# Performance work log

Measured on AMD Instinct MI355X. Metric: run time of the kernel, lower is better.

The kernel has to match this reference:

```python
import jax, jax.numpy as jnp
import numpy as np

B, T, HID = 1, 256, 2048
H, D = 16, 128
KD = H * D
CONV = 4
MAX_CG = 30
LAMB_LB = 0.25
NORM_EPS = 1e-5


def setup_inputs() -> dict:
    key = jax.random.key(0)
    ks = jax.random.split(key, 10)
    s = 0.02
    init_lamb = float(np.log(np.exp(1.0 - LAMB_LB) - 1.0))  # softplus^-1(1 - lower_bound)
    return {
        "hidden_states": jax.random.normal(ks[0], (B, T, HID), jnp.float32),
        "Wq": jax.random.normal(ks[1], (HID, KD), jnp.float32) * s,
        "Wk": jax.random.normal(ks[2], (HID, KD), jnp.float32) * s,
        "Wv": jax.random.normal(ks[3], (HID, KD), jnp.float32) * s,
        "Wa": jax.random.normal(ks[4], (HID, H), jnp.float32) * s,
        "ba": jnp.full((H,), 2.0, jnp.float32),
        "Wb": jax.random.normal(ks[5], (HID, H), jnp.float32) * s,
        "bb": jnp.zeros((H,), jnp.float32),
        "conv_wq": jax.random.normal(ks[6], (KD, CONV), jnp.float32) * s,
        "conv_wk": jax.random.normal(ks[7], (KD, CONV), jnp.float32) * s,
        "lambda_params": jnp.full((KD,), init_lamb, jnp.float32),
        "o_norm_w": jnp.ones((D,), jnp.float32),
        "Wo": jax.random.normal(ks[8], (KD, HID), jnp.float32) * s,
    }


def short_conv_silu(x, w):
    # depthwise causal conv over time; x [b,t,c], w [c,k]
    k = w.shape[1]
    xp = jnp.pad(x, ((0, 0), (k - 1, 0), (0, 0)))
    t = x.shape[1]
    y = xp[:, 0:t, :] * w[:, 0]
    for i in range(1, k):
        y = y + xp[:, i:i + t, :] * w[:, i]
    return jax.nn.silu(y)


def l2norm(x):
    return x * jax.lax.rsqrt(jnp.sum(x * x, -1, keepdims=True) + 1e-6)


def rmsnorm(x, w):
    return x * jax.lax.rsqrt(jnp.mean(x * x, -1, keepdims=True) + NORM_EPS) * w


def cg_solve(A, b):
    # solve A x = b per (batch, head) with fixed CG iterations, x0 = 0
    matvec = lambda p: jnp.einsum('bhij,bhj->bhi', A, p)
    x0 = jnp.zeros_like(b)
    rs0 = jnp.sum(b * b, -1)

    def body(i, st):
        xc, r, p, rs = st
        Ap = matvec(p)
        alpha = rs / (jnp.sum(p * Ap, -1) + 1e-12)
        xc = xc + alpha[..., None] * p
        r = r - alpha[..., None] * Ap
        rs_n = jnp.sum(r * r, -1)
        p = r + (rs_n / (rs + 1e-12))[..., None] * p
        return xc, r, p, rs_n

    xf, _, _, _ = jax.lax.fori_loop(0, MAX_CG, body, (x0, b, b, rs0))
    return xf


def mesa_recurrence(q, k, v, g, beta, lamb_diag):
    # q,k,v [b,t,h,d]; g,beta [b,t,h]; lamb_diag [h,d,d]
    def step(carry, inp):
        h_kk, h_kv = carry
        qt, kt, vt, gt, bt = inp
        decay = jnp.exp(gt)[..., None, None]
        b_ = bt[..., None, None]
        h_kk = h_kk * decay + b_ * (kt[..., :, None] * kt[..., None, :])
        h_kv = h_kv * decay + b_ * (kt[..., :, None] * vt[..., None, :])
        A = h_kk + lamb_diag[None]
        q_star = cg_solve(A, qt)
        ot = jnp.einsum('bhk,bhkv->bhv', q_star, h_kv)
        return (h_kk, h_kv), ot

    init = (jnp.zeros((B, H, D, D), q.dtype), jnp.zeros((B, H, D, D), q.dtype))
    xs = (q.transpose(1, 0, 2, 3), k.transpose(1, 0, 2, 3), v.transpose(1, 0, 2, 3),
          g.transpose(1, 0, 2), beta.transpose(1, 0, 2))
    _, o = jax.lax.scan(step, init, xs)
    return o.transpose(1, 0, 2, 3)  # [b,t,h,d]


def reference(hidden_states, Wq, Wk, Wv, Wa, ba, Wb, bb, conv_wq, conv_wk,
              lambda_params, o_norm_w, Wo):
    x = hidden_states
    q = short_conv_silu(x @ Wq, conv_wq)
    k = short_conv_silu(x @ Wk, conv_wk)
    v = x @ Wv
    q = l2norm(q.reshape(B, T, H, D))
    k = l2norm(k.reshape(B, T, H, D))
    v = v.reshape(B, T, H, D)
    beta = jax.nn.sigmoid(x @ Wb + bb)          # [b,t,h]
    g = jax.nn.log_sigmoid(x @ Wa + ba)          # [b,t,h]
    lamb = (jax.nn.softplus(lambda_params) + LAMB_LB).reshape(H, D)
    lamb_diag = lamb[:, :, None] * jnp.eye(D, dtype=lamb.dtype)  # [h,d,d]
    o = mesa_recurrence(q, k, v, g, beta, lamb_diag)
    o = rmsnorm(o, o_norm_w)
    o = o.reshape(B, T, KD) @ Wo
    return o
```

## Files before the change

kernel.cpp:

```cpp
#include <hip/hip_runtime.h>
#include <math.h>

#define TT 256
#define HIDDEN 2048
#define NH 16
#define HD 128
#define KDIM 2048
#define NCG 30

typedef _Float16 h4 __attribute__((ext_vector_type(4)));
typedef _Float16 half8 __attribute__((ext_vector_type(8)));
typedef float floatx4 __attribute__((ext_vector_type(4)));

__device__ __forceinline__ half8 cvt8(const float4 x, const float4 y) {
    half8 f;
    f[0] = (_Float16)x.x; f[1] = (_Float16)x.y; f[2] = (_Float16)x.z; f[3] = (_Float16)x.w;
    f[4] = (_Float16)y.x; f[5] = (_Float16)y.y; f[6] = (_Float16)y.z; f[7] = (_Float16)y.w;
    return f;
}

#define ASTR 72
__global__ __launch_bounds__(256) void gemm_kernel(
    const float* __restrict__ A,
    const float* __restrict__ Wq, const float* __restrict__ Wk,
    const float* __restrict__ Wv,
    const float* __restrict__ Wa, const float* __restrict__ Wb,
    float* __restrict__ C0, float* __restrict__ C1, float* __restrict__ C2,
    const float* __restrict__ ba, const float* __restrict__ bb,
    float* __restrict__ g, float* __restrict__ beta)
{
    __shared__ __align__(16) _Float16 Bsh[2][8192];
    __shared__ __align__(16) _Float16 Ash[2][32 * ASTR];

    const int tid = threadIdx.x, lane = tid & 63, w = tid >> 6;
    const int q = lane >> 4, l16 = lane & 15;

    const int b = blockIdx.x;
    const int xcd = b & 7, gslot = b >> 3;
    int nt, mt;
    if (gslot < 48) { nt = xcd * 6 + (gslot >> 3); mt = gslot & 7; }
    else           { nt = 48;                      mt = xcd; }
    const int mat = nt >> 4;
    const int ntile = nt & 15;
    const int n0 = ntile * 128;
    const float* __restrict__ W = (mat == 0) ? Wq : (mat == 1) ? Wk : (mat == 2) ? Wv : Wa;
    float* __restrict__ C = (mat == 0) ? C0 : (mat == 1) ? C1 : C2;
    const int m0 = mt * 32;
    const int kt2 = w >> 1;

    const int ar = tid >> 3, ac = (tid & 7) * 8;
    const float* __restrict__ Ap = &A[(size_t)(m0 + ar) * KDIM + ac];

    floatx4 acc[2][2] = {};
    float4 ax, ay;
    float bwv[2][16];
    float bab[16];

    auto loadB = [&](int s) {
        const float* base = &W[(size_t)(s * 64 + w * 16) * KDIM + n0 + lane];
#pragma unroll
        for (int i = 0; i < 16; i++) {
            bwv[0][i] = base[(size_t)i * KDIM];
            bwv[1][i] = base[(size_t)i * KDIM + 64];
        }
    };
    auto writeB = [&](int buf) {
#pragma unroll
        for (int hf = 0; hf < 2; hf++)
#pragma unroll
            for (int kg = 0; kg < 2; kg++) {
                const int kc = (w * 2 + kg) & 3;
                half8 h;
#pragma unroll
                for (int j = 0; j < 8; j++) h[j] = (_Float16)bwv[hf][kg * 8 + j];
                *(half8*)&Bsh[buf][((kt2 * 4 + kc) * 128 + hf * 64 + lane) * 8] = h;
            }
    };
    auto loadBab = [&](int s) {
        if (w >= 2) return;
        const float* __restrict__ Wsrc = (w == 0) ? Wa : Wb;
        const int hh = lane & 15, ko = lane >> 4;
#pragma unroll
        for (int hf = 0; hf < 2; hf++)
#pragma unroll
            for (int j = 0; j < 8; j++)
                bab[hf * 8 + j] = Wsrc[(size_t)(s * 64 + hf * 32 + ko * 8 + j) * NH + hh];
    };
    auto writeBab = [&](int buf) {
        if (w >= 2) return;
        const int hh = lane & 15, ko = lane >> 4;
        const int nn = w * 16 + hh;
#pragma unroll
        for (int hf = 0; hf < 2; hf++) {
            half8 h;
#pragma unroll
            for (int j = 0; j < 8; j++) h[j] = (_Float16)bab[hf * 8 + j];
            *(half8*)&Bsh[buf][((hf * 4 + ko) * 128 + nn) * 8] = h;
        }
    };

    if (mat == 3) {
        half8 z = {};
#pragma unroll
        for (int i = 0; i < 6; i++) {
            const int idx = i * 256 + tid;
            const int buf = idx & 1;
            const int rest = idx >> 1;
            const int slot = rest / 96, nrel = rest - slot * 96;
            *(half8*)&Bsh[buf][(slot * 128 + 32 + nrel) * 8] = z;
        }
        loadBab(0); writeBab(0); loadBab(1);
    } else {
        loadB(0); writeB(0); loadB(1);
    }
    ax = *(const float4*)&Ap[0]; ay = *(const float4*)&Ap[4];
    *(half8*)&Ash[0][ar * ASTR + ac] = cvt8(ax, ay);
    ax = *(const float4*)&Ap[64]; ay = *(const float4*)&Ap[68];
    __syncthreads();

    const int NSTEP = KDIM / 64;
    for (int s = 0; s < NSTEP; s++) {
        const int cur = s & 1;
#pragma unroll
        for (int kk = 0; kk < 2; kk++) {
            const half8 bf0 = *(const half8*)&Bsh[cur][kk * 4096 + q * 1024 + (w * 32 + l16) * 8];
            const half8 bf1 = *(const half8*)&Bsh[cur][kk * 4096 + q * 1024 + (w * 32 + 16 + l16) * 8];
            const half8 af0 = *(const half8*)&Ash[cur][l16 * ASTR + kk * 32 + q * 8];
            const half8 af1 = *(const half8*)&Ash[cur][(16 + l16) * ASTR + kk * 32 + q * 8];
            acc[0][0] = __builtin_amdgcn_mfma_f32_16x16x32_f16(af0, bf0, acc[0][0], 0, 0, 0);
            acc[0][1] = __builtin_amdgcn_mfma_f32_16x16x32_f16(af0, bf1, acc[0][1], 0, 0, 0);
            acc[1][0] = __builtin_amdgcn_mfma_f32_16x16x32_f16(af1, bf0, acc[1][0], 0, 0, 0);
            acc[1][1] = __builtin_amdgcn_mfma_f32_16x16x32_f16(af1, bf1, acc[1][1], 0, 0, 0);
        }
        if (s + 1 < NSTEP) {
            if (mat == 3) {
                writeBab(cur ^ 1);
                if (s + 2 < NSTEP) loadBab(s + 2);
            } else {
                writeB(cur ^ 1);
                if (s + 2 < NSTEP) loadB(s + 2);
            }
            *(half8*)&Ash[cur ^ 1][ar * ASTR + ac] = cvt8(ax, ay);
            if (s + 2 < NSTEP) {
                ax = *(const float4*)&Ap[(s + 2) * 64];
                ay = *(const float4*)&Ap[(s + 2) * 64 + 4];
            }
        }
        __syncthreads();
    }

    if (mat == 3) {
        if (w == 0) {
            const float bav = ba[l16], bbv = bb[l16];
#pragma unroll
            for (int r = 0; r < 4; r++) {
                const int t0r = m0 + q * 4 + r, t1r = m0 + 16 + q * 4 + r;
                float z0 = acc[0][0][r] + bav;
                g[t0r * NH + l16] = fminf(z0, 0.f) - log1pf(__expf(-fabsf(z0)));
                float z1 = acc[0][1][r] + bbv;
                beta[t0r * NH + l16] = 1.f / (1.f + __expf(-z1));
                float z2 = acc[1][0][r] + bav;
                g[t1r * NH + l16] = fminf(z2, 0.f) - log1pf(__expf(-fabsf(z2)));
                float z3 = acc[1][1][r] + bbv;
                beta[t1r * NH + l16] = 1.f / (1.f + __expf(-z3));
            }
        }
        return;
    }

#pragma unroll
    for (int r = 0; r < 4; r++) {
        C[(size_t)(m0 + q * 4 + r) * KDIM + n0 + w * 32 + l16] = acc[0][0][r];
        C[(size_t)(m0 + q * 4 + r) * KDIM + n0 + w * 32 + 16 + l16] = acc[0][1][r];
        C[(size_t)(m0 + 16 + q * 4 + r) * KDIM + n0 + w * 32 + l16] = acc[1][0][r];
        C[(size_t)(m0 + 16 + q * 4 + r) * KDIM + n0 + w * 32 + 16 + l16] = acc[1][1][r];
    }
}

__global__ __launch_bounds__(256) void gemm64_kernel(
    const float* __restrict__ A, const float* __restrict__ Wo,
    float* __restrict__ C)
{
    __shared__ __align__(16) _Float16 Bsh[2][4096];
    __shared__ __align__(16) _Float16 Ash[2][32 * ASTR];

    const int tid = threadIdx.x, lane = tid & 63, w = tid >> 6;
    const int q = lane >> 4, l16 = lane & 15;
    const int b = blockIdx.x;
    const int xcd = b & 7, gslot = b >> 3;
    const int nt = xcd * 4 + (gslot >> 3), mt = gslot & 7;
    const int n0 = nt * 64, m0 = mt * 32;
    const int kt2 = w >> 1;

    const int ar = tid >> 3, ac = (tid & 7) * 8;
    const float* __restrict__ Ap = &A[(size_t)(m0 + ar) * KDIM + ac];

    floatx4 acc0 = {}, acc1 = {};
    float4 ax, ay;
    float bwv[16];

    auto loadB = [&](int s) {
        const float* base = &Wo[(size_t)(s * 64 + w * 16) * KDIM + n0 + lane];
#pragma unroll
        for (int i = 0; i < 16; i++) bwv[i] = base[(size_t)i * KDIM];
    };
    auto writeB = [&](int buf) {
#pragma unroll
        for (int kg = 0; kg < 2; kg++) {
            const int kc = (w * 2 + kg) & 3;
            half8 h;
#pragma unroll
            for (int j = 0; j < 8; j++) h[j] = (_Float16)bwv[kg * 8 + j];
            *(half8*)&Bsh[buf][((kt2 * 4 + kc) * 64 + lane) * 8] = h;
        }
    };

    loadB(0); writeB(0); loadB(1);
    ax = *(const float4*)&Ap[0]; ay = *(const float4*)&Ap[4];
    *(half8*)&Ash[0][ar * ASTR + ac] = cvt8(ax, ay);
    ax = *(const float4*)&Ap[64]; ay = *(const float4*)&Ap[68];
    __syncthreads();

    const int NSTEP = KDIM / 64;
    for (int s = 0; s < NSTEP; s++) {
        const int cur = s & 1;
#pragma unroll
        for (int kk = 0; kk < 2; kk++) {
            const half8 bf  = *(const half8*)&Bsh[cur][kk * 2048 + q * 512 + (w * 16 + l16) * 8];
            const half8 af0 = *(const half8*)&Ash[cur][l16 * ASTR + kk * 32 + q * 8];
            const half8 af1 = *(const half8*)&Ash[cur][(16 + l16) * ASTR + kk * 32 + q * 8];
            acc0 = __builtin_amdgcn_mfma_f32_16x16x32_f16(af0, bf, acc0, 0, 0, 0);
            acc1 = __builtin_amdgcn_mfma_f32_16x16x32_f16(af1, bf, acc1, 0, 0, 0);
        }
        if (s + 1 < NSTEP) {
            writeB(cur ^ 1);
            if (s + 2 < NSTEP) loadB(s + 2);
            *(half8*)&Ash[cur ^ 1][ar * ASTR + ac] = cvt8(ax, ay);
            if (s + 2 < NSTEP) {
                ax = *(const float4*)&Ap[(s + 2) * 64];
                ay = *(const float4*)&Ap[(s + 2) * 64 + 4];
            }
        }
        __syncthreads();
    }

#pragma unroll
    for (int r = 0; r < 4; r++) {
        C[(size_t)(m0 + q * 4 + r) * KDIM + n0 + w * 16 + l16] = acc0[r];
        C[(size_t)(m0 + 16 + q * 4 + r) * KDIM + n0 + w * 16 + l16] = acc1[r];
    }
}

__global__ __launch_bounds__(256) void conv_silu_l2_kernel(
    const float* __restrict__ q_pre, const float* __restrict__ k_pre,
    const float* __restrict__ cwq, const float* __restrict__ cwk,
    float* __restrict__ qn, float* __restrict__ kn)
{
    const int t = blockIdx.x, h = blockIdx.y;
    const int which = threadIdx.x >> 7, d = threadIdx.x & 127;
    const int w = threadIdx.x >> 6;
    const int c = h * HD + d;
    const float* pre = which ? k_pre : q_pre;
    const float* cw  = which ? cwk : cwq;
    float y = 0.f;
#pragma unroll
    for (int i = 0; i < 4; i++) {
        const int ts = t - 3 + i;
        if (ts >= 0) y = fmaf(pre[ts * KDIM + c], cw[c * 4 + i], y);
    }
    const float s = y / (1.f + __expf(-y));
    float v = s * s;
#pragma unroll
    for (int off = 32; off > 0; off >>= 1) v += __shfl_down(v, off, 64);
    __shared__ float red[4];
    if ((threadIdx.x & 63) == 0) red[w] = v;
    __syncthreads();
    const float sum = red[which * 2] + red[which * 2 + 1];
    float* dst = which ? kn : qn;
    dst[t * KDIM + c] = s * rsqrtf(sum + 1e-6f);
}

#define PSTR 136
#define YSTR 264

template<int SMAX>
__device__ __forceinline__ void mesa_cg(
    const float* __restrict__ qn, const float* __restrict__ kn, const float* __restrict__ vv,
    const float* __restrict__ g, const float* __restrict__ bet, const float* __restrict__ lp,
    const float* __restrict__ onw, float* __restrict__ out,
    int h, int t0, _Float16* Psh, _Float16* Ysh, float* red,
    float* Gsh, float* bets)
{
    constexpr int NSUB1 = SMAX / 64;
    constexpr int NK2   = SMAX / 32;

    const int tid = threadIdx.x, lane = tid & 63, w = tid >> 6;
    const int quad = lane >> 4, l16 = lane & 15;
    const int tmy = t0 + l16;
    const int dbase = w * 32;

    {
        float sc = g[tid * NH + h];
#pragma unroll
        for (int off = 1; off < 64; off <<= 1) {
            const float o = __shfl_up(sc, off, 64);
            if (lane >= off) sc += o;
        }
        if (lane == 63) red[w] = sc;
        bets[tid] = bet[tid * NH + h];
        __syncthreads();
        float woff = 0.f;
        for (int u = 0; u < w; u++) woff += red[u];
        Gsh[tid] = sc + woff;
        __syncthreads();
    }

    half8 K1[NSUB1][4];
#pragma unroll
    for (int ii = 0; ii < NSUB1; ii++) {
        const int srow = 16 * (w + 4 * ii) + l16;
        const float* kp = &kn[(srow * NH + h) * HD];
#pragma unroll
        for (int kk = 0; kk < 4; kk++) {
            const float4 a = *(const float4*)&kp[kk * 32 + quad * 8];
            const float4 b = *(const float4*)&kp[kk * 32 + quad * 8 + 4];
            K1[ii][kk] = cvt8(a, b);
        }
    }

    half8 KtF[2][NK2];
#pragma unroll
    for (int ss = 0; ss < 2; ss++) {
        const int d = dbase + ss * 16 + l16;
#pragma unroll
        for (int kk = 0; kk < NK2; kk++) {
#pragma unroll
            for (int j = 0; j < 8; j++) {
                const int s = kk * 32 + quad * 8 + j;
                KtF[ss][kk][j] = (_Float16)kn[(s * NH + h) * HD + d];
            }
        }
    }

    half8 Vf[NK2][2];
#pragma unroll
    for (int kk = 0; kk < NK2; kk++) {
#pragma unroll
        for (int ss = 0; ss < 2; ss++) {
            const int dv = dbase + ss * 16 + l16;
#pragma unroll
            for (int j = 0; j < 8; j++) {
                const int s = kk * 32 + quad * 8 + j;
                Vf[kk][ss][j] = (_Float16)vv[(s * NH + h) * HD + dv];
            }
        }
    }

    const float Gt = Gsh[tmy];
    float Wm[NSUB1][4];
#pragma unroll
    for (int ii = 0; ii < NSUB1; ii++)
#pragma unroll
        for (int r = 0; r < 4; r++) {
            const int s = 16 * (w + 4 * ii) + quad * 4 + r;
            Wm[ii][r] = (s <= tmy) ? bets[s] * __expf(Gt - Gsh[s]) : 0.f;
        }
    float lam[8], xv[8], rv[8], pv[8];
#pragma unroll
    for (int ss = 0; ss < 2; ss++)
#pragma unroll
        for (int r = 0; r < 4; r++) {
            const int e = ss * 4 + r;
            const int d = dbase + ss * 16 + quad * 4 + r;
            const float lx = lp[h * HD + d];
            lam[e] = fmaxf(lx, 0.f) + log1pf(__expf(-fabsf(lx))) + 0.25f;
            const float b = qn[(tmy * NH + h) * HD + d];
            xv[e] = 0.f; rv[e] = b; pv[e] = b;
        }
    float rs = 0.f;
#pragma unroll
    for (int e = 0; e < 8; e++) rs += rv[e] * rv[e];
    rs += __shfl_xor(rs, 16, 64); rs += __shfl_xor(rs, 32, 64);

    auto writeP = [&](const float* src) {
#pragma unroll
        for (int ss = 0; ss < 2; ss++) {
            h4 ph;
            ph.x = (_Float16)src[ss * 4 + 0]; ph.y = (_Float16)src[ss * 4 + 1];
            ph.z = (_Float16)src[ss * 4 + 2]; ph.w = (_Float16)src[ss * 4 + 3];
            *(h4*)&Psh[l16 * PSTR + dbase + ss * 16 + quad * 4] = ph;
        }
    };
    writeP(pv);

    for (int it = 0; it <= NCG; it++) {
        __syncthreads();
        floatx4 acc1a[NSUB1] = {}, acc1b[NSUB1] = {};
#pragma unroll
        for (int kk = 0; kk < 2; kk++) {
            const half8 bfa = *(const half8*)&Psh[l16 * PSTR + kk * 32 + quad * 8];
            const half8 bfb = *(const half8*)&Psh[l16 * PSTR + (kk + 2) * 32 + quad * 8];
#pragma unroll
            for (int ii = 0; ii < NSUB1; ii++) {
                acc1a[ii] = __builtin_amdgcn_mfma_f32_16x16x32_f16(K1[ii][kk], bfa, acc1a[ii], 0, 0, 0);
                acc1b[ii] = __builtin_amdgcn_mfma_f32_16x16x32_f16(K1[ii][kk + 2], bfb, acc1b[ii], 0, 0, 0);
            }
        }
#pragma unroll
        for (int ii = 0; ii < NSUB1; ii++) {
            h4 yh;
            yh.x = (_Float16)(Wm[ii][0] * (acc1a[ii][0] + acc1b[ii][0]));
            yh.y = (_Float16)(Wm[ii][1] * (acc1a[ii][1] + acc1b[ii][1]));
            yh.z = (_Float16)(Wm[ii][2] * (acc1a[ii][2] + acc1b[ii][2]));
            yh.w = (_Float16)(Wm[ii][3] * (acc1a[ii][3] + acc1b[ii][3]));
            *(h4*)&Ysh[l16 * YSTR + 16 * (w + 4 * ii) + quad * 4] = yh;
        }
        __syncthreads();
        if (it == NCG) break;

        floatx4 acc2a[2] = {}, acc2b[2] = {};
#pragma unroll
        for (int kk = 0; kk < NK2; kk += 2) {
            const half8 bf0 = *(const half8*)&Ysh[l16 * YSTR + kk * 32 + quad * 8];
            const half8 bf1 = *(const half8*)&Ysh[l16 * YSTR + (kk + 1) * 32 + quad * 8];
#pragma unroll
            for (int ss = 0; ss < 2; ss++) {
                acc2a[ss] = __builtin_amdgcn_mfma_f32_16x16x32_f16(KtF[ss][kk], bf0, acc2a[ss], 0, 0, 0);
                acc2b[ss] = __builtin_amdgcn_mfma_f32_16x16x32_f16(KtF[ss][kk + 1], bf1, acc2b[ss], 0, 0, 0);
            }
        }
        float Ap[8], pAp = 0.f;
#pragma unroll
        for (int ss = 0; ss < 2; ss++)
#pragma unroll
            for (int r = 0; r < 4; r++) {
                const int e = ss * 4 + r;
                Ap[e] = (acc2a[ss][r] + acc2b[ss][r]) + lam[e] * pv[e];
                pAp = fmaf(pv[e], Ap[e], pAp);
            }
        pAp += __shfl_xor(pAp, 16, 64); pAp += __shfl_xor(pAp, 32, 64);
        const float alpha = rs / (pAp + 1e-12f);
        float rsn = 0.f;
#pragma unroll
        for (int e = 0; e < 8; e++) {
            xv[e] = fmaf(alpha, pv[e], xv[e]);
            rv[e] = fmaf(-alpha, Ap[e], rv[e]);
            rsn = fmaf(rv[e], rv[e], rsn);
        }
        rsn += __shfl_xor(rsn, 16, 64); rsn += __shfl_xor(rsn, 32, 64);
        const float bcg = rsn / (rs + 1e-12f);
#pragma unroll
        for (int e = 0; e < 8; e++) pv[e] = fmaf(bcg, pv[e], rv[e]);
        rs = rsn;
        writeP(it == NCG - 1 ? xv : pv);
    }

    floatx4 accOa[2] = {}, accOb[2] = {};
#pragma unroll
    for (int kk = 0; kk < NK2; kk += 2) {
        const half8 af0 = *(const half8*)&Ysh[l16 * YSTR + kk * 32 + quad * 8];
        const half8 af1 = *(const half8*)&Ysh[l16 * YSTR + (kk + 1) * 32 + quad * 8];
#pragma unroll
        for (int ss = 0; ss < 2; ss++) {
            accOa[ss] = __builtin_amdgcn_mfma_f32_16x16x32_f16(af0, Vf[kk][ss], accOa[ss], 0, 0, 0);
            accOb[ss] = __builtin_amdgcn_mfma_f32_16x16x32_f16(af1, Vf[kk + 1][ss], accOb[ss], 0, 0, 0);
        }
    }
    float accO[2][4];
#pragma unroll
    for (int ss = 0; ss < 2; ss++)
#pragma unroll
        for (int r = 0; r < 4; r++) accO[ss][r] = accOa[ss][r] + accOb[ss][r];

    float part[4];
#pragma unroll
    for (int r = 0; r < 4; r++) {
        part[r] = accO[0][r] * accO[0][r] + accO[1][r] * accO[1][r];
#pragma unroll
        for (int off = 1; off < 16; off <<= 1) part[r] += __shfl_xor(part[r], off, 64);
    }
    if (l16 == 0) {
#pragma unroll
        for (int r = 0; r < 4; r++) red[w * 16 + quad * 4 + r] = part[r];
    }
    __syncthreads();
    const float w0 = onw[dbase + l16], w1 = onw[dbase + 16 + l16];
#pragma unroll
    for (int r = 0; r < 4; r++) {
        const int qr = quad * 4 + r;
        const float sumd = red[qr] + red[16 + qr] + red[32 + qr] + red[48 + qr];
        const float sc = rsqrtf(sumd * (1.f / HD) + 1e-5f);
        const int trow = ((t0 + qr) * NH + h) * HD;
        out[trow + dbase + l16] = accO[0][r] * sc * w0;
        out[trow + dbase + 16 + l16] = accO[1][r] * sc * w1;
    }
}

__global__ __launch_bounds__(256, 1) void mesa_kernel(
    const float* __restrict__ qn, const float* __restrict__ kn, const float* __restrict__ vv,
    const float* __restrict__ g, const float* __restrict__ bet, const float* __restrict__ lp,
    const float* __restrict__ onw, float* __restrict__ out)
{
    __shared__ __align__(16) _Float16 Psh[16 * PSTR];
    __shared__ __align__(16) _Float16 Ysh[16 * YSTR];
    __shared__ float red[64];
    __shared__ float Gsh[256];
    __shared__ float bets[256];
    const int h = blockIdx.x, jb = blockIdx.y, t0 = jb * 16;
    switch (jb >> 2) {
        case 0:  mesa_cg<64> (qn, kn, vv, g, bet, lp, onw, out, h, t0, Psh, Ysh, red, Gsh, bets); break;
        case 1:  mesa_cg<128>(qn, kn, vv, g, bet, lp, onw, out, h, t0, Psh, Ysh, red, Gsh, bets); break;
        case 2:  mesa_cg<192>(qn, kn, vv, g, bet, lp, onw, out, h, t0, Psh, Ysh, red, Gsh, bets); break;
        default: mesa_cg<256>(qn, kn, vv, g, bet, lp, onw, out, h, t0, Psh, Ysh, red, Gsh, bets); break;
    }
}

extern "C" void kernel_launch(void* const* d_in, const int* in_sizes, int n_in,
                              void* d_out, int out_size, void* d_ws, size_t ws_size,
                              hipStream_t stream)
{
    (void)in_sizes; (void)n_in; (void)out_size; (void)ws_size;
    const float* x   = (const float*)d_in[0];
    const float* Wq  = (const float*)d_in[1];
    const float* Wk  = (const float*)d_in[2];
    const float* Wv  = (const float*)d_in[3];
    const float* Wa  = (const float*)d_in[4];
    const float* ba  = (const float*)d_in[5];
    const float* Wb  = (const float*)d_in[6];
    const float* bb  = (const float*)d_in[7];
    const float* cwq = (const float*)d_in[8];
    const float* cwk = (const float*)d_in[9];
    const float* lp  = (const float*)d_in[10];
    const float* onw = (const float*)d_in[11];
    const float* Wo  = (const float*)d_in[12];

    char* wsb = (char*)d_ws;
    float* q_pre = (float*)wsb;
    float* k_pre = q_pre + 524288;
    float* v     = k_pre + 524288;
    float* qn    = v + 524288;
    float* kn    = qn + 524288;
    float* g     = kn + 524288;
    float* beta  = g + 4096;
    float* onorm = q_pre;
    float* outp  = (float*)d_out;

    gemm_kernel<<<dim3(392), 256, 0, stream>>>(x, Wq, Wk, Wv, Wa, Wb,
                                               q_pre, k_pre, v, ba, bb, g, beta);
    conv_silu_l2_kernel<<<dim3(TT, NH), 256, 0, stream>>>(q_pre, k_pre, cwq, cwk, qn, kn);

    mesa_kernel<<<dim3(NH, 16), 256, 0, stream>>>(qn, kn, v, g, beta, lp, onw, onorm);

    gemm64_kernel<<<dim3(256), 256, 0, stream>>>(onorm, Wo, outp);
}
```

Baseline: 222.4 us.

## Stage GEMM weight tiles with direct global-to-LDS loads in fp32

Both projection GEMMs now copy weight tiles straight from global memory into shared memory as fp32 using global_load_lds. This replaces the register round-trip and pre-conversion to fp16, and the staging is issued one step ahead. Conversion to fp16 moves to the fragment-read side, which now does strided scalar LDS reads. LDS use for the main GEMM doubles and needs a dynamic-shared-memory attribute, which may lower occupancy and add bank conflicts.

```diff
diff --git a/kernel.cpp b/kernel.cpp
--- a/kernel.cpp
+++ b/kernel.cpp
@@ -19,7 +19,15 @@
     return f;
 }
 
+__device__ __forceinline__ void glds16(const void* g, void* l) {
+    __builtin_amdgcn_global_load_lds(
+        (const __attribute__((address_space(1))) void*)g,
+        (__attribute__((address_space(3))) void*)l, 16, 0, 0);
+}
+
 #define ASTR 72
+#define GEMM_LDS (2 * 64 * 128 * 4 + 2 * 32 * ASTR * 2)
+
 __global__ __launch_bounds__(256) void gemm_kernel(
     const float* __restrict__ A,
     const float* __restrict__ Wq, const float* __restrict__ Wk,
@@ -29,8 +37,9 @@
     const float* __restrict__ ba, const float* __restrict__ bb,
     float* __restrict__ g, float* __restrict__ beta)
 {
-    __shared__ __align__(16) _Float16 Bsh[2][8192];
-    __shared__ __align__(16) _Float16 Ash[2][32 * ASTR];
+    extern __shared__ char smem[];
+    float* Bf = (float*)smem;
+    _Float16* Ash = (_Float16*)(smem + 65536);
 
     const int tid = threadIdx.x, lane = tid & 63, w = tid >> 6;
     const int q = lane >> 4, l16 = lane & 15;
@@ -46,35 +55,22 @@
     const float* __restrict__ W = (mat == 0) ? Wq : (mat == 1) ? Wk : (mat == 2) ? Wv : Wa;
     float* __restrict__ C = (mat == 0) ? C0 : (mat == 1) ? C1 : C2;
     const int m0 = mt * 32;
-    const int kt2 = w >> 1;
 
     const int ar = tid >> 3, ac = (tid & 7) * 8;
     const float* __restrict__ Ap = &A[(size_t)(m0 + ar) * KDIM + ac];
 
     floatx4 acc[2][2] = {};
     float4 ax, ay;
-    float bwv[2][16];
     float bab[16];
 
-    auto loadB = [&](int s) {
-        const float* base = &W[(size_t)(s * 64 + w * 16) * KDIM + n0 + lane];
-#pragma unroll
-        for (int i = 0; i < 16; i++) {
-            bwv[0][i] = base[(size_t)i * KDIM];
-            bwv[1][i] = base[(size_t)i * KDIM + 64];
-        }
-    };
-    auto writeB = [&](int buf) {
-#pragma unroll
-        for (int hf = 0; hf < 2; hf++)
-#pragma unroll
-            for (int kg = 0; kg < 2; kg++) {
-                const int kc = (w * 2 + kg) & 3;
-                half8 h;
-#pragma unroll
-                for (int j = 0; j < 8; j++) h[j] = (_Float16)bwv[hf][kg * 8 + j];
-                *(half8*)&Bsh[buf][((kt2 * 4 + kc) * 128 + hf * 64 + lane) * 8] = h;
-            }
+    auto stageB = [&](int s, int buf) {
+#pragma unroll
+        for (int i = 0; i < 8; i++) {
+            const int r0 = w * 16 + i * 2;
+            const int row = r0 + (lane >> 5);
+            glds16(&W[(size_t)(s * 64 + row) * KDIM + n0 + (lane & 31) * 4],
+                   &Bf[(buf * 64 + r0) * 128]);
+        }
     };
     auto loadBab = [&](int s) {
         if (w >= 2) return;
@@ -89,44 +85,48 @@
     auto writeBab = [&](int buf) {
         if (w >= 2) return;
         const int hh = lane & 15, ko = lane >> 4;
-        const int nn = w * 16 + hh;
-#pragma unroll
-        for (int hf = 0; hf < 2; hf++) {
-            half8 h;
-#pragma unroll
-            for (int j = 0; j < 8; j++) h[j] = (_Float16)bab[hf * 8 + j];
-            *(half8*)&Bsh[buf][((hf * 4 + ko) * 128 + nn) * 8] = h;
-        }
+        const int col = w * 16 + hh;
+#pragma unroll
+        for (int hf = 0; hf < 2; hf++)
+#pragma unroll
+            for (int j = 0; j < 8; j++)
+                Bf[(buf * 64 + hf * 32 + ko * 8 + j) * 128 + col] = bab[hf * 8 + j];
     };
 
     if (mat == 3) {
-        half8 z = {};
-#pragma unroll
-        for (int i = 0; i < 6; i++) {
-            const int idx = i * 256 + tid;
-            const int buf = idx & 1;
-            const int rest = idx >> 1;
-            const int slot = rest / 96, nrel = rest - slot * 96;
-            *(half8*)&Bsh[buf][(slot * 128 + 32 + nrel) * 8] = z;
+        for (int i = tid; i < 2 * 64 * 96; i += 256) {
+            const int buf = i / 6144;
+            const int rest = i - buf * 6144;
+            const int row = rest / 96, col = 32 + (rest - row * 96);
+            Bf[(buf * 64 + row) * 128 + col] = 0.f;
         }
         loadBab(0); writeBab(0); loadBab(1);
     } else {
-        loadB(0); writeB(0); loadB(1);
+        stageB(0, 0);
     }
     ax = *(const float4*)&Ap[0]; ay = *(const float4*)&Ap[4];
-    *(half8*)&Ash[0][ar * ASTR + ac] = cvt8(ax, ay);
+    *(half8*)&Ash[ar * ASTR + ac] = cvt8(ax, ay);
     ax = *(const float4*)&Ap[64]; ay = *(const float4*)&Ap[68];
     __syncthreads();
 
     const int NSTEP = KDIM / 64;
     for (int s = 0; s < NSTEP; s++) {
         const int cur = s & 1;
+        if (mat != 3 && s + 1 < NSTEP)
+            stageB(s + 1, cur ^ 1);
 #pragma unroll
         for (int kk = 0; kk < 2; kk++) {
-            const half8 bf0 = *(const half8*)&Bsh[cur][kk * 4096 + q * 1024 + (w * 32 + l16) * 8];
-            const half8 bf1 = *(const half8*)&Bsh[cur][kk * 4096 + q * 1024 + (w * 32 + 16 + l16) * 8];
-            const half8 af0 = *(const half8*)&Ash[cur][l16 * ASTR + kk * 32 + q * 8];
-            const half8 af1 = *(const half8*)&Ash[cur][(16 + l16) * ASTR + kk * 32 + q * 8];
+            float f0[8], f1[8];
+#pragma unroll
+            for (int j = 0; j < 8; j++) {
+                const int rowb = (cur * 64 + kk * 32 + q * 8 + j) * 128 + w * 32 + l16;
+                f0[j] = Bf[rowb];
+                f1[j] = Bf[rowb + 16];
+            }
+            const half8 bf0 = cvt8(*(const float4*)&f0[0], *(const float4*)&f0[4]);
+            const half8 bf1 = cvt8(*(const float4*)&f1[0], *(const float4*)&f1[4]);
+            const half8 af0 = *(const half8*)&Ash[cur * 32 * ASTR + l16 * ASTR + kk * 32 + q * 8];
+            const half8 af1 = *(const half8*)&Ash[cur * 32 * ASTR + (16 + l16) * ASTR + kk * 32 + q * 8];
             acc[0][0] = __builtin_amdgcn_mfma_f32_16x16x32_f16(af0, bf0, acc[0][0], 0, 0, 0);
             acc[0][1] = __builtin_amdgcn_mfma_f32_16x16x32_f16(af0, bf1, acc[0][1], 0, 0, 0);
             acc[1][0] = __builtin_amdgcn_mfma_f32_16x16x32_f16(af1, bf0, acc[1][0], 0, 0, 0);
@@ -136,11 +136,8 @@
             if (mat == 3) {
                 writeBab(cur ^ 1);
                 if (s + 2 < NSTEP) loadBab(s + 2);
-            } else {
-                writeB(cur ^ 1);
-                if (s + 2 < NSTEP) loadB(s + 2);
-            }
-            *(half8*)&Ash[cur ^ 1][ar * ASTR + ac] = cvt8(ax, ay);
+            }
+            *(half8*)&Ash[(cur ^ 1) * 32 * ASTR + ar * ASTR + ac] = cvt8(ax, ay);
             if (s + 2 < NSTEP) {
                 ax = *(const float4*)&Ap[(s + 2) * 64];
                 ay = *(const float4*)&Ap[(s + 2) * 64 + 4];
@@ -181,7 +178,7 @@
     const float* __restrict__ A, const float* __restrict__ Wo,
     float* __restrict__ C)
 {
-    __shared__ __align__(16) _Float16 Bsh[2][4096];
+    __shared__ __align__(16) float Bf[2][64][64];
     __shared__ __align__(16) _Float16 Ash[2][32 * ASTR];
 
     const int tid = threadIdx.x, lane = tid & 63, w = tid >> 6;
@@ -190,32 +187,24 @@
     const int xcd = b & 7, gslot = b >> 3;
     const int nt = xcd * 4 + (gslot >> 3), mt = gslot & 7;
     const int n0 = nt * 64, m0 = mt * 32;
-    const int kt2 = w >> 1;
 
     const int ar = tid >> 3, ac = (tid & 7) * 8;
     const float* __restrict__ Ap = &A[(size_t)(m0 + ar) * KDIM + ac];
 
     floatx4 acc0 = {}, acc1 = {};
     float4 ax, ay;
-    float bwv[16];
-
-    auto loadB = [&](int s) {
-        const float* base = &Wo[(size_t)(s * 64 + w * 16) * KDIM + n0 + lane];
-#pragma unroll
-        for (int i = 0; i < 16; i++) bwv[i] = base[(size_t)i * KDIM];
+
+    auto stageB = [&](int s, int buf) {
+#pragma unroll
+        for (int i = 0; i < 4; i++) {
+            const int r0 = w * 16 + i * 4;
+            const int row = r0 + (lane >> 4);
+            glds16(&Wo[(size_t)(s * 64 + row) * KDIM + n0 + (lane & 15) * 4],
+                   &Bf[buf][r0][0]);
+        }
     };
-    auto writeB = [&](int buf) {
-#pragma unroll
-        for (int kg = 0; kg < 2; kg++) {
-            const int kc = (w * 2 + kg) & 3;
-            half8 h;
-#pragma unroll
-            for (int j = 0; j < 8; j++) h[j] = (_Float16)bwv[kg * 8 + j];
-            *(half8*)&Bsh[buf][((kt2 * 4 + kc) * 64 + lane) * 8] = h;
-        }
-    };
-
-    loadB(0); writeB(0); loadB(1);
+
+    stageB(0, 0);
     ax = *(const float4*)&Ap[0]; ay = *(const float4*)&Ap[4];
     *(half8*)&Ash[0][ar * ASTR + ac] = cvt8(ax, ay);
     ax = *(const float4*)&Ap[64]; ay = *(const float4*)&Ap[68];
@@ -224,17 +213,20 @@
     const int NSTEP = KDIM / 64;
     for (int s = 0; s < NSTEP; s++) {
         const int cur = s & 1;
+        if (s + 1 < NSTEP) stageB(s + 1, cur ^ 1);
 #pragma unroll
         for (int kk = 0; kk < 2; kk++) {
-            const half8 bf  = *(const half8*)&Bsh[cur][kk * 2048 + q * 512 + (w * 16 + l16) * 8];
+            float f[8];
+#pragma unroll
+            for (int j = 0; j < 8; j++)
+                f[j] = Bf[cur][kk * 32 + q * 8 + j][w * 16 + l16];
+            const half8 bf  = cvt8(*(const float4*)&f[0], *(const float4*)&f[4]);
             const half8 af0 = *(const half8*)&Ash[cur][l16 * ASTR + kk * 32 + q * 8];
             const half8 af1 = *(const half8*)&Ash[cur][(16 + l16) * ASTR + kk * 32 + q * 8];
             acc0 = __builtin_amdgcn_mfma_f32_16x16x32_f16(af0, bf, acc0, 0, 0, 0);
             acc1 = __builtin_amdgcn_mfma_f32_16x16x32_f16(af1, bf, acc1, 0, 0, 0);
         }
         if (s + 1 < NSTEP) {
-            writeB(cur ^ 1);
-            if (s + 2 < NSTEP) loadB(s + 2);
             *(half8*)&Ash[cur ^ 1][ar * ASTR + ac] = cvt8(ax, ay);
             if (s + 2 < NSTEP) {
                 ax = *(const float4*)&Ap[(s + 2) * 64];
@@ -545,8 +537,10 @@
     float* onorm = q_pre;
     float* outp  = (float*)d_out;
 
-    gemm_kernel<<<dim3(392), 256, 0, stream>>>(x, Wq, Wk, Wv, Wa, Wb,
-                                               q_pre, k_pre, v, ba, bb, g, beta);
+    (void)hipFuncSetAttribute((const void*)gemm_kernel,
+                              hipFuncAttributeMaxDynamicSharedMemorySize, GEMM_LDS);
+    gemm_kernel<<<dim3(392), 256, GEMM_LDS, stream>>>(x, Wq, Wk, Wv, Wa, Wb,
+                                                      q_pre, k_pre, v, ba, bb, g, beta);
     conv_silu_l2_kernel<<<dim3(TT, NH), 256, 0, stream>>>(q_pre, k_pre, cwq, cwk, qn, kn);
 
     mesa_kernel<<<dim3(NH, 16), 256, 0, stream>>>(qn, kn, v, g, beta, lp, onw, onorm);
```

After: 224.8 us. Within noise of the previous version (+1.1%).
